# Kernel optimization log

Hardware: AMD Instinct MI355X
Metric: run time of the kernel (lower is better)

The kernel has to match this reference:

```python
import jax, jax.numpy as jnp
import numpy as np

G, NB, C, K, R, S = 5, 5, 64, 3, 8, 2   # n_groups, n_blocks, n_feats, kernel, reduction, scale
MOCO = 256


def setup_inputs() -> dict:
    key = jax.random.key(0)
    ks = iter(jax.random.split(key, 32))
    def rn(shape, s=0.02):
        return jax.random.normal(next(ks), shape, jnp.float32) * s
    return {
        "x": jax.random.normal(next(ks), (16, 3, 64, 64), jnp.float32),
        "k_v": jax.random.normal(next(ks), (16, MOCO), jnp.float32),
        "head_w": rn((C, 3, K, K)), "head_b": rn((C,)),
        "comp_w": rn((C, MOCO)),
        # DA_conv params, stacked over [group, block, which-of-2]
        "da_kw1": rn((G, NB, 2, C, C)),
        "da_kw2": rn((G, NB, 2, C * K * K, C)),
        "da_cw": rn((G, NB, 2, C, C)), "da_cb": rn((G, NB, 2, C)),
        "ca_w1": rn((G, NB, 2, C // R, C)), "ca_w2": rn((G, NB, 2, C, C // R)),
        # DAB plain 3x3 convs (conv1, conv2)
        "dab_cw": rn((G, NB, 2, C, C, K, K)), "dab_cb": rn((G, NB, 2, C)),
        # per-group tail conv, body tail conv, upsampler, final conv
        "grp_w": rn((G, C, C, K, K)), "grp_b": rn((G, C)),
        "body_w": rn((C, C, K, K)), "body_b": rn((C,)),
        "up_w": rn((C * S * S, C, K, K)), "up_b": rn((C * S * S,)),
        "tail_w": rn((3, C, K, K)), "tail_b": rn((3,)),
    }


def lrelu(x):
    return jax.nn.leaky_relu(x, 0.1)


def conv2d(x, w, b):
    p = (K - 1) // 2
    y = jax.lax.conv_general_dilated(x, w, (1, 1), [(p, p), (p, p)],
                                     dimension_numbers=("NCHW", "OIHW", "NCHW"))
    return y + b[None, :, None, None]


def da_conv(x, kv, kw1, kw2, cw, cb, caw1, caw2):
    # x: [B,C,H,W], kv: [B,C]
    B, Ch, H, W = x.shape
    # per-sample, per-channel dynamic KxK kernel (torch: groups=B*C depthwise conv)
    ker = (lrelu(kv @ kw1.T) @ kw2.T).reshape(B, Ch, K, K)
    p = (K - 1) // 2
    xp = jnp.pad(x, ((0, 0), (0, 0), (p, p), (p, p)))
    out = jnp.zeros_like(x)
    for i in range(K):
        for j in range(K):
            out = out + ker[:, :, i, j, None, None] * xp[:, :, i:i + H, j:j + W]
    out = lrelu(out)
    # 1x1 conv (with bias)
    out = jnp.einsum("bchw,oc->bohw", out, cw) + cb[None, :, None, None]
    # CA gate on kv (two bias-free 1x1 convs on 1x1 spatial == matmuls)
    att = jax.nn.sigmoid(lrelu(kv @ caw1.T) @ caw2.T)  # [B,C]
    return out + x * att[:, :, None, None]


def pixel_shuffle(t, r):
    B, Ct, H, W = t.shape
    c = Ct // (r * r)
    return t.reshape(B, c, r, r, H, W).transpose(0, 1, 4, 2, 5, 3).reshape(B, c, H * r, W * r)


def _forward(x, k_v, head_w, head_b, comp_w, da_kw1, da_kw2, da_cw, da_cb,
             ca_w1, ca_w2, dab_cw, dab_cb, grp_w, grp_b, body_w, body_b,
             up_w, up_b, tail_w, tail_b):
    kv = lrelu(k_v @ comp_w.T)            # compress: [B, C]
    x0 = conv2d(x, head_w, head_b)        # head
    res = x0
    for g in range(G):                    # DAGs
        gin = res
        for n in range(NB):               # DABs
            bin_ = res
            out = lrelu(da_conv(res, kv, da_kw1[g, n, 0], da_kw2[g, n, 0],
                                da_cw[g, n, 0], da_cb[g, n, 0], ca_w1[g, n, 0], ca_w2[g, n, 0]))
            out = lrelu(conv2d(out, dab_cw[g, n, 0], dab_cb[g, n, 0]))
            out = lrelu(da_conv(out, kv, da_kw1[g, n, 1], da_kw2[g, n, 1],
                                da_cw[g, n, 1], da_cb[g, n, 1], ca_w1[g, n, 1], ca_w2[g, n, 1]))
            res = conv2d(out, dab_cw[g, n, 1], dab_cb[g, n, 1]) + bin_
        res = conv2d(res, grp_w[g], grp_b[g]) + gin
    res = conv2d(res, body_w, body_b) + x0
    t = pixel_shuffle(conv2d(res, up_w, up_b), S)   # Upsampler (scale=2)
    return conv2d(t, tail_w, tail_b)


def reference(x, k_v, head_w, head_b, comp_w, da_kw1, da_kw2, da_cw, da_cb,
              ca_w1, ca_w2, dab_cw, dab_cb, grp_w, grp_b, body_w, body_b,
              up_w, up_b, tail_w, tail_b):
    return _forward(x, k_v, head_w, head_b, comp_w, da_kw1, da_kw2, da_cw, da_cb,
                    ca_w1, ca_w2, dab_cw, dab_cb, grp_w, grp_b, body_w, body_b,
                    up_w, up_b, tail_w, tail_b)
```

## Files before the change

kernel.cpp:

```cpp
#include <hip/hip_runtime.h>
#include <math.h>

#define DEV __device__ __forceinline__

DEV float lrelu_f(float v) { return v > 0.f ? v : 0.1f * v; }

DEV unsigned short f2bf(float f) {
    unsigned u = __builtin_bit_cast(unsigned, f);
    unsigned r = u + 0x7FFFu + ((u >> 16) & 1u);
    return (unsigned short)(r >> 16);
}

DEV float bf2f(unsigned short s) {
    return __builtin_bit_cast(float, (unsigned)s << 16);
}

typedef __attribute__((ext_vector_type(8))) short bh8;
typedef __attribute__((ext_vector_type(16))) float f16acc;

#define MFMA32(acc, a, b) acc = __builtin_amdgcn_mfma_f32_32x32x16_bf16(a, b, acc, 0, 0, 0)

__global__ void transpose_w(const float* __restrict__ src, float* __restrict__ dst,
                            int L, int O, int KK) {
    int idx = blockIdx.x * 256 + threadIdx.x;
    int tot = L * O * KK;
    if (idx >= tot) return;
    int l = idx / (O * KK);
    int r = idx - l * (O * KK);
    int o = r / KK;
    int k = r - o * KK;
    dst[((size_t)l * KK + k) * O + o] = src[idx];
}

__global__ void pack3x3(const float* __restrict__ src, unsigned short* __restrict__ dst, int L) {
    int idx = blockIdx.x * 256 + threadIdx.x;
    if (idx >= L * 4608) return;
    int l = idx / 4608;
    int r = idx - l * 4608;
    int c = r >> 7;
    int rr = r & 127;
    int nt = rr >> 6, lane = rr & 63;
    int o = nt * 32 + (lane & 31);
    int kg = lane >> 5;
    unsigned short v[8];
#pragma unroll
    for (int j = 0; j < 8; ++j) {
        int k = c * 16 + kg * 8 + j;
        int t = k >> 6, cin = k & 63;
        v[j] = f2bf(src[(((size_t)l * 64 + o) * 64 + cin) * 9 + t]);
    }
    uint4 u;
    u.x = v[0] | ((unsigned)v[1] << 16);
    u.y = v[2] | ((unsigned)v[3] << 16);
    u.z = v[4] | ((unsigned)v[5] << 16);
    u.w = v[6] | ((unsigned)v[7] << 16);
    *(uint4*)(dst + (size_t)idx * 8) = u;
}

__global__ void pack_da(const float* __restrict__ src, unsigned short* __restrict__ dst, int L) {
    int idx = blockIdx.x * 256 + threadIdx.x;
    if (idx >= L * 512) return;
    int l = idx >> 9;
    int r = idx & 511;
    int c = r >> 7;
    int rr = r & 127;
    int nt = rr >> 6, lane = rr & 63;
    int o = nt * 32 + (lane & 31);
    int kg = lane >> 5;
    unsigned short v[8];
#pragma unroll
    for (int j = 0; j < 8; ++j) {
        int cin = c * 16 + kg * 8 + j;
        v[j] = f2bf(src[((size_t)l * 64 + o) * 64 + cin]);
    }
    uint4 u;
    u.x = v[0] | ((unsigned)v[1] << 16);
    u.y = v[2] | ((unsigned)v[3] << 16);
    u.z = v[4] | ((unsigned)v[5] << 16);
    u.w = v[6] | ((unsigned)v[7] << 16);
    *(uint4*)(dst + (size_t)idx * 8) = u;
}

__global__ void pack_up(const float* __restrict__ src, unsigned short* __restrict__ dst) {
    int idx = blockIdx.x * 256 + threadIdx.x;
    if (idx >= 18432) return;
    int c = idx >> 9;
    int nt = (idx >> 6) & 7;
    int lane = idx & 63;
    int o = nt * 32 + (lane & 31);
    int kg = lane >> 5;
    unsigned short v[8];
#pragma unroll
    for (int j = 0; j < 8; ++j) {
        int k = c * 16 + kg * 8 + j;
        int t = k >> 6, cin = k & 63;
        v[j] = f2bf(src[((size_t)o * 64 + cin) * 9 + t]);
    }
    uint4 u;
    u.x = v[0] | ((unsigned)v[1] << 16);
    u.y = v[2] | ((unsigned)v[3] << 16);
    u.z = v[4] | ((unsigned)v[5] << 16);
    u.w = v[6] | ((unsigned)v[7] << 16);
    *(uint4*)(dst + (size_t)idx * 8) = u;
}

__global__ void pack_tail(const float* __restrict__ src, unsigned short* __restrict__ dst) {
    int idx = blockIdx.x * 256 + threadIdx.x;
    if (idx >= 2304) return;
    int c = idx >> 6;
    int lane = idx & 63;
    int o = lane & 31;
    int kg = lane >> 5;
    unsigned short v[8];
#pragma unroll
    for (int j = 0; j < 8; ++j) {
        int k = c * 16 + kg * 8 + j;
        int t = k >> 6, cin = k & 63;
        v[j] = (o < 3) ? f2bf(src[((size_t)o * 64 + cin) * 9 + t]) : (unsigned short)0;
    }
    uint4 u;
    u.x = v[0] | ((unsigned)v[1] << 16);
    u.y = v[2] | ((unsigned)v[3] << 16);
    u.z = v[4] | ((unsigned)v[5] << 16);
    u.w = v[6] | ((unsigned)v[7] << 16);
    *(uint4*)(dst + (size_t)idx * 8) = u;
}

__global__ void kv_kernel(const float* __restrict__ kvin, const float* __restrict__ comp_w,
                          float* __restrict__ kv) {
    int b = blockIdx.x, c = threadIdx.x;
    const float* a = kvin + b * 256;
    const float* w = comp_w + c * 256;
    float s = 0.f;
    for (int m = 0; m < 256; ++m) s += a[m] * w[m];
    kv[b * 64 + c] = lrelu_f(s);
}

__global__ void kerprep(const float* __restrict__ kv, const float* __restrict__ kw1,
                        const float* __restrict__ kw2, const float* __restrict__ caw1,
                        const float* __restrict__ caw2, float* __restrict__ ker_all,
                        float* __restrict__ att_all) {
    int l = blockIdx.x >> 4;
    int b = blockIdx.x & 15;
    int c = threadIdx.x;
    __shared__ float kvb[64];
    __shared__ float t1[64];
    __shared__ float a1[8];
    kvb[c] = kv[b * 64 + c];
    __syncthreads();
    {
        const float* w1 = kw1 + (size_t)l * 4096 + c * 64;
        float s = 0.f;
        for (int j = 0; j < 64; ++j) s += kvb[j] * w1[j];
        t1[c] = lrelu_f(s);
    }
    if (c < 8) {
        const float* cw1 = caw1 + (size_t)l * 512 + c * 64;
        float s = 0.f;
        for (int j = 0; j < 64; ++j) s += kvb[j] * cw1[j];
        a1[c] = lrelu_f(s);
    }
    __syncthreads();
    const float* w2 = kw2 + (size_t)l * 576 * 64;
    for (int t = 0; t < 9; ++t) {
        const float* row = w2 + (size_t)(c * 9 + t) * 64;
        float s = 0.f;
        for (int j = 0; j < 64; ++j) s += t1[j] * row[j];
        ker_all[(((size_t)l * 16 + b) * 9 + t) * 64 + c] = s;
    }
    {
        const float* c2 = caw2 + (size_t)l * 512 + c * 8;
        float s = 0.f;
        for (int r = 0; r < 8; ++r) s += a1[r] * c2[r];
        att_all[((size_t)l * 16 + b) * 64 + c] = 1.f / (1.f + expf(-s));
    }
}

__global__ __launch_bounds__(256) void head_conv(const float* __restrict__ x,
                                                 const float* __restrict__ wt,
                                                 const float* __restrict__ bias,
                                                 float* __restrict__ x0,
                                                 float* __restrict__ res,
                                                 unsigned short* __restrict__ resS) {
    int t = threadIdx.x;
    int co = t & 63, q = t >> 6;
    int bid = blockIdx.x;
    int b = bid >> 7;
    int rem = bid & 127;
    int y = rem >> 1;
    int xs = (rem & 1) * 32 + q * 8;

    float bv = bias[co];
    float acc[8];
#pragma unroll
    for (int p = 0; p < 8; ++p) acc[p] = bv;

    int coff[10];
    bool cok[10];
#pragma unroll
    for (int i = 0; i < 10; ++i) {
        int col = xs - 1 + i;
        cok[i] = (col >= 0) && (col < 64);
        coff[i] = cok[i] ? col : 0;
    }
    for (int cin = 0; cin < 3; ++cin) {
#pragma unroll
        for (int ky = 0; ky < 3; ++ky) {
            int row = y + ky - 1;
            bool rok = (row >= 0) && (row < 64);
            const float* rp = x + ((size_t)(b * 3 + cin) * 64 + (rok ? row : 0)) * 64;
            float v[10];
#pragma unroll
            for (int i = 0; i < 10; ++i) v[i] = (rok && cok[i]) ? rp[coff[i]] : 0.f;
            const float* wp = wt + ((cin * 3 + ky) * 3) * 64 + co;
            float w0 = wp[0], w1 = wp[64], w2 = wp[128];
#pragma unroll
            for (int p = 0; p < 8; ++p) acc[p] += w0 * v[p] + w1 * v[p + 1] + w2 * v[p + 2];
        }
    }
    size_t ob = (((size_t)b * 64 + y) * 64 + xs) * 64 + co;
#pragma unroll
    for (int p = 0; p < 8; ++p) {
        x0[ob + (size_t)p * 64] = acc[p];
        res[ob + (size_t)p * 64] = acc[p];
        resS[ob + (size_t)p * 64] = f2bf(acc[p]);
    }
}

__global__ __launch_bounds__(256, 2) void conv3x3_mfma(const unsigned short* __restrict__ in,
                                                       const unsigned short* __restrict__ wp,
                                                       const float* __restrict__ bias,
                                                       const float* __restrict__ residF,
                                                       float* __restrict__ outF,
                                                       unsigned short* __restrict__ outB,
                                                       int act) {
    __shared__ unsigned short sm[180 * 72];
    int tid = threadIdx.x;
    int bid = blockIdx.x;
    int b = bid >> 5;
    int rem = bid & 31;
    int ty = rem >> 2, tx = rem & 3;
    const unsigned short* inb = in + (size_t)b * 262144;

    int lane = tid & 63, w = tid >> 6;
    const unsigned short* bp = wp + (size_t)lane * 8;

    bh8 q0[6], q1[6];
#pragma unroll
    for (int i = 0; i < 6; ++i) {
        q0[i] = *(const bh8*)&bp[(size_t)i * 1024];
        q1[i] = *(const bh8*)&bp[(size_t)i * 1024 + 512];
    }

    for (int i = tid; i < 1440; i += 256) {
        int px = i >> 3, c8 = i & 7;
        int hy = px / 18, hx = px - hy * 18;
        int row = ty * 8 + hy - 1, col = tx * 16 + hx - 1;
        uint4 u = make_uint4(0u, 0u, 0u, 0u);
        if (row >= 0 && row < 64 && col >= 0 && col < 64)
            u = *(const uint4*)(inb + (((size_t)row * 64 + col) * 64 + c8 * 8));
        *(uint4*)&sm[px * 72 + c8 * 8] = u;
    }
    __syncthreads();

    int l31 = lane & 31, kg8 = (lane >> 5) * 8;
    int p0 = w * 32 + l31;
    int ly0 = p0 >> 4, lx0 = p0 & 15;

    f16acc a0 = {0,0,0,0,0,0,0,0,0,0,0,0,0,0,0,0};
    f16acc a1 = a0;

#pragma unroll
    for (int c = 0; c < 36; ++c) {
        int t = c >> 2, cc = c & 3;
        int tyt = t / 3, txt = t - tyt * 3;
        int base = ((ly0 + tyt) * 18 + lx0 + txt) * 72 + cc * 16 + kg8;
        bh8 A = *(const bh8*)&sm[base];
        bh8 B0 = q0[c % 6], B1 = q1[c % 6];
        if (c + 6 < 36) {
            q0[c % 6] = *(const bh8*)&bp[(size_t)(c + 6) * 1024];
            q1[c % 6] = *(const bh8*)&bp[(size_t)(c + 6) * 1024 + 512];
        }
        MFMA32(a0, A, B0);
        MFMA32(a1, A, B1);
    }

    float bias0 = bias[l31], bias1 = bias[32 + l31];
    int hi = lane >> 5;
    size_t outb = (size_t)b * 262144;
#pragma unroll
    for (int r = 0; r < 16; ++r) {
        int rowm = (r & 3) + 8 * (r >> 2) + 4 * hi;
        int m = w * 32 + rowm;
        int gy = ty * 8 + (m >> 4), gx = tx * 16 + (m & 15);
        size_t i0 = outb + (((size_t)gy * 64 + gx) * 64);
        float v0 = a0[r] + bias0, v1 = a1[r] + bias1;
        if (residF) {
            v0 += residF[i0 + l31];
            v1 += residF[i0 + 32 + l31];
        }
        if (act) { v0 = lrelu_f(v0); v1 = lrelu_f(v1); }
        if (outF) {
            outF[i0 + l31] = v0;
            outF[i0 + 32 + l31] = v1;
        }
        if (outB) {
            outB[i0 + l31] = f2bf(v0);
            outB[i0 + 32 + l31] = f2bf(v1);
        }
    }
}

__global__ __launch_bounds__(256, 2) void da_mfma(const unsigned short* __restrict__ in,
                                                  const unsigned short* __restrict__ wp,
                                                  const float* __restrict__ cb,
                                                  const float* __restrict__ kerT,
                                                  const float* __restrict__ attv,
                                                  unsigned short* __restrict__ out) {
    __shared__ unsigned short sm[180 * 72];
    __shared__ unsigned short mid[128 * 72];
    __shared__ unsigned short bds[4096];
    int tid = threadIdx.x;
    int bid = blockIdx.x;
    int b = bid >> 5;
    int rem = bid & 31;
    int ty = rem >> 2, tx = rem & 3;
    const unsigned short* inb = in + (size_t)b * 262144;

    for (int i = tid; i < 1440; i += 256) {
        int px = i >> 3, c8 = i & 7;
        int hy = px / 18, hx = px - hy * 18;
        int row = ty * 8 + hy - 1, col = tx * 16 + hx - 1;
        uint4 u = make_uint4(0u, 0u, 0u, 0u);
        if (row >= 0 && row < 64 && col >= 0 && col < 64)
            u = *(const uint4*)(inb + (((size_t)row * 64 + col) * 64 + c8 * 8));
        *(uint4*)&sm[px * 72 + c8 * 8] = u;
    }
#pragma unroll
    for (int i = 0; i < 2; ++i) {
        int idx = i * 256 + tid;
        *(uint4*)&bds[idx * 8] = *(const uint4*)&wp[idx * 8];
    }
    __syncthreads();

    {
        int c2 = tid & 31, q = tid >> 5;
        const float* kb = kerT + (size_t)b * 576 + 2 * c2;
        float ka[9], kbv[9];
#pragma unroll
        for (int t = 0; t < 9; ++t) {
            ka[t] = kb[t * 64];
            kbv[t] = kb[t * 64 + 1];
        }
        float m0[16], m1[16];
#pragma unroll
        for (int xx = 0; xx < 16; ++xx) { m0[xx] = 0.f; m1[xx] = 0.f; }
#pragma unroll
        for (int ky = 0; ky < 3; ++ky) {
            int hr = q + ky;
            float va[18], vb[18];
#pragma unroll
            for (int i = 0; i < 18; ++i) {
                unsigned u = *(const unsigned*)&sm[(hr * 18 + i) * 72 + 2 * c2];
                va[i] = bf2f((unsigned short)(u & 0xffffu));
                vb[i] = bf2f((unsigned short)(u >> 16));
            }
            float k0a = ka[ky * 3], k1a = ka[ky * 3 + 1], k2a = ka[ky * 3 + 2];
            float k0b = kbv[ky * 3], k1b = kbv[ky * 3 + 1], k2b = kbv[ky * 3 + 2];
#pragma unroll
            for (int xx = 0; xx < 16; ++xx) {
                m0[xx] += k0a * va[xx] + k1a * va[xx + 1] + k2a * va[xx + 2];
                m1[xx] += k0b * vb[xx] + k1b * vb[xx + 1] + k2b * vb[xx + 2];
            }
        }
#pragma unroll
        for (int xx = 0; xx < 16; ++xx) {
            unsigned u = (unsigned)f2bf(lrelu_f(m0[xx])) |
                         ((unsigned)f2bf(lrelu_f(m1[xx])) << 16);
            *(unsigned*)&mid[(q * 16 + xx) * 72 + 2 * c2] = u;
        }
    }
    __syncthreads();

    int lane = tid & 63, w = tid >> 6;
    int l31 = lane & 31, kg8 = (lane >> 5) * 8;
    int base = (w * 32 + l31) * 72 + kg8;

    f16acc a0 = {0,0,0,0,0,0,0,0,0,0,0,0,0,0,0,0};
    f16acc a1 = a0;
#pragma unroll
    for (int cc = 0; cc < 4; ++cc) {
        bh8 A = *(const bh8*)&mid[base + cc * 16];
        bh8 B0 = *(const bh8*)&bds[((cc * 2 + 0) * 64 + lane) * 8];
        bh8 B1 = *(const bh8*)&bds[((cc * 2 + 1) * 64 + lane) * 8];
        MFMA32(a0, A, B0);
        MFMA32(a1, A, B1);
    }

    float cb0 = cb[l31], cb1 = cb[32 + l31];
    float at0 = attv[b * 64 + l31], at1 = attv[b * 64 + 32 + l31];
    int hi = lane >> 5;
    size_t outb = (size_t)b * 262144;
#pragma unroll
    for (int r = 0; r < 16; ++r) {
        int rowm = (r & 3) + 8 * (r >> 2) + 4 * hi;
        int m = w * 32 + rowm;
        int gy = ty * 8 + (m >> 4), gx = tx * 16 + (m & 15);
        size_t i0 = outb + (((size_t)gy * 64 + gx) * 64);
        float v0 = a0[r] + cb0 + bf2f(in[i0 + l31]) * at0;
        float v1 = a1[r] + cb1 + bf2f(in[i0 + 32 + l31]) * at1;
        out[i0 + l31] = f2bf(lrelu_f(v0));
        out[i0 + 32 + l31] = f2bf(lrelu_f(v1));
    }
}

__global__ __launch_bounds__(256, 2) void up_mfma(const unsigned short* __restrict__ in,
                                                  const unsigned short* __restrict__ wp,
                                                  const float* __restrict__ bias,
                                                  unsigned short* __restrict__ shuf) {
    __shared__ unsigned short sm[100 * 72];
    int tid = threadIdx.x;
    int bid = blockIdx.x;
    int b = bid >> 6;
    int t6 = bid & 63;
    int ty = t6 >> 3, tx = t6 & 7;
    const unsigned short* inb = in + (size_t)b * 262144;

    int lane = tid & 63, w = tid >> 6;
    const unsigned short* bp = wp + (size_t)(w * 2) * 512 + (size_t)lane * 8;

    bh8 q0[4], q1[4];
#pragma unroll
    for (int i = 0; i < 4; ++i) {
        q0[i] = *(const bh8*)&bp[(size_t)i * 4096];
        q1[i] = *(const bh8*)&bp[(size_t)i * 4096 + 512];
    }

    for (int i = tid; i < 800; i += 256) {
        int px = i >> 3, c8 = i & 7;
        int hy = px / 10, hx = px - hy * 10;
        int row = ty * 8 + hy - 1, col = tx * 8 + hx - 1;
        uint4 u = make_uint4(0u, 0u, 0u, 0u);
        if (row >= 0 && row < 64 && col >= 0 && col < 64)
            u = *(const uint4*)(inb + (((size_t)row * 64 + col) * 64 + c8 * 8));
        *(uint4*)&sm[px * 72 + c8 * 8] = u;
    }
    __syncthreads();

    int l31 = lane & 31, kg8 = (lane >> 5) * 8;
    int ly0 = l31 >> 3, lx0 = l31 & 7;

    f16acc a00 = {0,0,0,0,0,0,0,0,0,0,0,0,0,0,0,0};
    f16acc a01 = a00, a10 = a00, a11 = a00;

#pragma unroll
    for (int c = 0; c < 36; ++c) {
        int t = c >> 2, cc = c & 3;
        int tyt = t / 3, txt = t - tyt * 3;
        int base0 = ((ly0 + tyt) * 10 + lx0 + txt) * 72 + cc * 16 + kg8;
        int base1 = base0 + 2880;
        bh8 A0 = *(const bh8*)&sm[base0];
        bh8 A1 = *(const bh8*)&sm[base1];
        bh8 B0 = q0[c % 4], B1 = q1[c % 4];
        if (c + 4 < 36) {
            q0[c % 4] = *(const bh8*)&bp[(size_t)(c + 4) * 4096];
            q1[c % 4] = *(const bh8*)&bp[(size_t)(c + 4) * 4096 + 512];
        }
        MFMA32(a00, A0, B0);
        MFMA32(a01, A0, B1);
        MFMA32(a10, A1, B0);
        MFMA32(a11, A1, B1);
    }

    int co0 = w * 64 + l31, co1 = co0 + 32;
    float bias0 = bias[co0], bias1 = bias[co1];
    int ch0 = co0 >> 2, r10 = (co0 >> 1) & 1, r20 = co0 & 1;
    int ch1 = co1 >> 2, r11 = (co1 >> 1) & 1, r21 = co1 & 1;
    int hi = lane >> 5;
#pragma unroll
    for (int r = 0; r < 16; ++r) {
        int rowm = (r & 3) + 8 * (r >> 2) + 4 * hi;
#pragma unroll
        for (int mt = 0; mt < 2; ++mt) {
            int m = mt * 32 + rowm;
            int y = ty * 8 + (m >> 3), x = tx * 8 + (m & 7);
            float va = (mt == 0) ? a00[r] : a10[r];
            float vb = (mt == 0) ? a01[r] : a11[r];
            shuf[(((size_t)b * 128 + 2 * y + r10) * 128 + 2 * x + r20) * 64 + ch0] = f2bf(va + bias0);
            shuf[(((size_t)b * 128 + 2 * y + r11) * 128 + 2 * x + r21) * 64 + ch1] = f2bf(vb + bias1);
        }
    }
}

__global__ __launch_bounds__(256) void tail_mfma(const unsigned short* __restrict__ shuf,
                                                 const unsigned short* __restrict__ wp,
                                                 const float* __restrict__ bias,
                                                 float* __restrict__ outp) {
    __shared__ unsigned short sm[324 * 72];
    int tid = threadIdx.x;
    int bid = blockIdx.x;
    int b = bid >> 6;
    int rem = bid & 63;
    int ty = rem >> 3, tx = rem & 7;
    const unsigned short* sb = shuf + (size_t)b * 128 * 128 * 64;

    for (int i = tid; i < 2592; i += 256) {
        int px = i >> 3, c8 = i & 7;
        int hy = px / 18, hx = px - hy * 18;
        int row = ty * 16 + hy - 1, col = tx * 16 + hx - 1;
        uint4 u = make_uint4(0u, 0u, 0u, 0u);
        if (row >= 0 && row < 128 && col >= 0 && col < 128)
            u = *(const uint4*)(sb + (((size_t)row * 128 + col) * 64 + c8 * 8));
        *(uint4*)&sm[px * 72 + c8 * 8] = u;
    }
    __syncthreads();

    int lane = tid & 63, w = tid >> 6;
    int l31 = lane & 31, kg8 = (lane >> 5) * 8;
    int mbase = w * 64;
    int p0 = mbase + l31;
    int ly0 = p0 >> 4, lx0 = p0 & 15;

    f16acc a0 = {0,0,0,0,0,0,0,0,0,0,0,0,0,0,0,0};
    f16acc a1 = a0;

#pragma unroll
    for (int t = 0; t < 9; ++t) {
        int tyt = t / 3, txt = t - tyt * 3;
        int base0 = ((ly0 + tyt) * 18 + lx0 + txt) * 72 + kg8;
        int base1 = base0 + 2592;
#pragma unroll
        for (int cc = 0; cc < 4; ++cc) {
            int c = t * 4 + cc;
            bh8 A0 = *(const bh8*)&sm[base0 + cc * 16];
            bh8 A1 = *(const bh8*)&sm[base1 + cc * 16];
            bh8 B = *(const bh8*)&wp[((size_t)c * 64 + lane) * 8];
            MFMA32(a0, A0, B);
            MFMA32(a1, A1, B);
        }
    }

    if (l31 < 3) {
        float bv = bias[l31];
        int hi = lane >> 5;
        size_t ob = ((size_t)b * 3 + l31) * 16384;
#pragma unroll
        for (int r = 0; r < 16; ++r) {
            int rowm = (r & 3) + 8 * (r >> 2) + 4 * hi;
            int m0 = mbase + rowm;
            int gy0 = ty * 16 + (m0 >> 4), gx0 = tx * 16 + (m0 & 15);
            outp[ob + (size_t)gy0 * 128 + gx0] = a0[r] + bv;
            int m1 = m0 + 32;
            int gy1 = ty * 16 + (m1 >> 4), gx1 = tx * 16 + (m1 & 15);
            outp[ob + (size_t)gy1 * 128 + gx1] = a1[r] + bv;
        }
    }
}

extern "C" void kernel_launch(void* const* d_in, const int* in_sizes, int n_in,
                              void* d_out, int out_size, void* d_ws, size_t ws_size,
                              hipStream_t stream) {
    const float* x      = (const float*)d_in[0];
    const float* k_v    = (const float*)d_in[1];
    const float* head_w = (const float*)d_in[2];
    const float* head_b = (const float*)d_in[3];
    const float* comp_w = (const float*)d_in[4];
    const float* da_kw1 = (const float*)d_in[5];
    const float* da_kw2 = (const float*)d_in[6];
    const float* da_cw  = (const float*)d_in[7];
    const float* da_cb  = (const float*)d_in[8];
    const float* ca_w1  = (const float*)d_in[9];
    const float* ca_w2  = (const float*)d_in[10];
    const float* dab_cw = (const float*)d_in[11];
    const float* dab_cb = (const float*)d_in[12];
    const float* grp_w  = (const float*)d_in[13];
    const float* grp_b  = (const float*)d_in[14];
    const float* body_w = (const float*)d_in[15];
    const float* body_b = (const float*)d_in[16];
    const float* up_w   = (const float*)d_in[17];
    const float* up_b   = (const float*)d_in[18];
    const float* tail_w = (const float*)d_in[19];
    const float* tail_b = (const float*)d_in[20];

    char* base = (char*)d_ws;
    auto alloc = [&](size_t bytes) -> char* {
        char* p = base;
        base += (bytes + 255) & ~(size_t)255;
        return p;
    };
    unsigned short* wp_dab  = (unsigned short*)alloc((size_t)50 * 36864 * 2);
    unsigned short* wp_grp  = (unsigned short*)alloc((size_t)5 * 36864 * 2);
    unsigned short* wp_body = (unsigned short*)alloc((size_t)36864 * 2);
    unsigned short* wp_up   = (unsigned short*)alloc((size_t)147456 * 2);
    unsigned short* wp_da   = (unsigned short*)alloc((size_t)50 * 4096 * 2);
    unsigned short* wp_tail = (unsigned short*)alloc((size_t)18432 * 2);
    float* wT_head = (float*)alloc(1728 * 4);
    float* kvbuf   = (float*)alloc(1024 * 4);
    float* ker_all = (float*)alloc((size_t)460800 * 4);
    float* att_all = (float*)alloc((size_t)51200 * 4);
    const size_t ACT = (size_t)16 * 64 * 64 * 64;
    float* x0 = (float*)alloc(ACT * 4);
    float* rA = (float*)alloc(ACT * 4);
    float* rB = (float*)alloc(ACT * 4);
    float* rC = (float*)alloc(ACT * 4);
    unsigned short* sA = (unsigned short*)alloc(ACT * 2);
    unsigned short* sB = (unsigned short*)alloc(ACT * 2);
    unsigned short* sC = (unsigned short*)alloc(ACT * 2);
    unsigned short* t0 = (unsigned short*)alloc(ACT * 2);
    unsigned short* t1 = (unsigned short*)alloc(ACT * 2);
    unsigned short* shuf = (unsigned short*)alloc((size_t)16 * 128 * 128 * 64 * 2);

    pack3x3<<<900, 256, 0, stream>>>(dab_cw, wp_dab, 50);
    pack3x3<<<90, 256, 0, stream>>>(grp_w, wp_grp, 5);
    pack3x3<<<18, 256, 0, stream>>>(body_w, wp_body, 1);
    pack_da<<<100, 256, 0, stream>>>(da_cw, wp_da, 50);
    pack_up<<<72, 256, 0, stream>>>(up_w, wp_up);
    pack_tail<<<9, 256, 0, stream>>>(tail_w, wp_tail);
    transpose_w<<<7, 256, 0, stream>>>(head_w, wT_head, 1, 64, 27);

    kv_kernel<<<16, 64, 0, stream>>>(k_v, comp_w, kvbuf);
    kerprep<<<800, 64, 0, stream>>>(kvbuf, da_kw1, da_kw2, ca_w1, ca_w2, ker_all, att_all);

    head_conv<<<2048, 256, 0, stream>>>(x, wT_head, head_b, x0, rA, sA);

    for (int g = 0; g < 5; ++g) {
        float* curF = rA;
        unsigned short* curS = sA;
        for (int n = 0; n < 5; ++n) {
            int l0 = (g * 5 + n) * 2, l1 = l0 + 1;
            da_mfma<<<512, 256, 0, stream>>>(curS, wp_da + (size_t)l0 * 4096,
                                             da_cb + (size_t)l0 * 64, ker_all + (size_t)l0 * 9216,
                                             att_all + (size_t)l0 * 1024, t0);
            conv3x3_mfma<<<512, 256, 0, stream>>>(t0, wp_dab + (size_t)l0 * 36864,
                                                  dab_cb + (size_t)l0 * 64, nullptr,
                                                  nullptr, t1, 1);
            da_mfma<<<512, 256, 0, stream>>>(t1, wp_da + (size_t)l1 * 4096,
                                             da_cb + (size_t)l1 * 64, ker_all + (size_t)l1 * 9216,
                                             att_all + (size_t)l1 * 1024, t0);
            float* outF = (curF == rB) ? rC : rB;
            unsigned short* outS = (curS == sB) ? sC : sB;
            conv3x3_mfma<<<512, 256, 0, stream>>>(t0, wp_dab + (size_t)l1 * 36864,
                                                  dab_cb + (size_t)l1 * 64, curF,
                                                  outF, outS, 0);
            curF = outF;
            curS = outS;
        }
        conv3x3_mfma<<<512, 256, 0, stream>>>(curS, wp_grp + (size_t)g * 36864,
                                              grp_b + (size_t)g * 64, rA, rC, sC, 0);
        float* tf = rA; rA = rC; rC = tf;
        unsigned short* ts = sA; sA = sC; sC = ts;
    }
    conv3x3_mfma<<<512, 256, 0, stream>>>(sA, wp_body, body_b, x0, nullptr, t0, 0);

    up_mfma<<<1024, 256, 0, stream>>>(t0, wp_up, up_b, shuf);
    tail_mfma<<<1024, 256, 0, stream>>>(shuf, wp_tail, tail_b, (float*)d_out);
}
```

Measured before the change: 1.534 ms.

## Fuse dynamic depthwise DA conv with following 3x3 conv into one kernel

Merges the da_mfma kernel and the subsequent conv3x3_mfma into a single dab_mfma kernel. It loads a 2-pixel halo tile and computes the DA output over an 18x10 halo region in shared memory, then runs the 3x3 MFMA conv directly from LDS. This removes one global write and read of the intermediate bf16 activation and one launch per DA/conv pair. The cost is redundant halo computation (180 vs 128 pixels), larger LDS use and more registers for the prefetched weights.

```diff
diff --git a/kernel.cpp b/kernel.cpp
--- a/kernel.cpp
+++ b/kernel.cpp
@@ -311,15 +311,19 @@
     }
 }
 
-__global__ __launch_bounds__(256, 2) void da_mfma(const unsigned short* __restrict__ in,
-                                                  const unsigned short* __restrict__ wp,
-                                                  const float* __restrict__ cb,
-                                                  const float* __restrict__ kerT,
-                                                  const float* __restrict__ attv,
-                                                  unsigned short* __restrict__ out) {
-    __shared__ unsigned short sm[180 * 72];
-    __shared__ unsigned short mid[128 * 72];
-    __shared__ unsigned short bds[4096];
+__global__ __launch_bounds__(256, 2) void dab_mfma(const unsigned short* __restrict__ in,
+                                                   const unsigned short* __restrict__ wda,
+                                                   const float* __restrict__ cb,
+                                                   const float* __restrict__ kerT,
+                                                   const float* __restrict__ attv,
+                                                   const unsigned short* __restrict__ wconv,
+                                                   const float* __restrict__ cbias,
+                                                   const float* __restrict__ residF,
+                                                   float* __restrict__ outF,
+                                                   unsigned short* __restrict__ outB,
+                                                   int act) {
+    __shared__ unsigned short sin_[240 * 72];
+    __shared__ unsigned short mid[192 * 72];
     int tid = threadIdx.x;
     int bid = blockIdx.x;
     int b = bid >> 5;
@@ -327,19 +331,24 @@
     int ty = rem >> 2, tx = rem & 3;
     const unsigned short* inb = in + (size_t)b * 262144;
 
-    for (int i = tid; i < 1440; i += 256) {
+    int lane = tid & 63, w = tid >> 6;
+    int l31 = lane & 31, kg8 = (lane >> 5) * 8, hi = lane >> 5;
+
+    bh8 dB0[4], dB1[4];
+#pragma unroll
+    for (int cc = 0; cc < 4; ++cc) {
+        dB0[cc] = *(const bh8*)&wda[((size_t)(cc * 2 + 0) * 64 + lane) * 8];
+        dB1[cc] = *(const bh8*)&wda[((size_t)(cc * 2 + 1) * 64 + lane) * 8];
+    }
+
+    for (int i = tid; i < 1920; i += 256) {
         int px = i >> 3, c8 = i & 7;
-        int hy = px / 18, hx = px - hy * 18;
-        int row = ty * 8 + hy - 1, col = tx * 16 + hx - 1;
+        int hy = px / 20, hx = px - hy * 20;
+        int row = ty * 8 + hy - 2, col = tx * 16 + hx - 2;
         uint4 u = make_uint4(0u, 0u, 0u, 0u);
         if (row >= 0 && row < 64 && col >= 0 && col < 64)
             u = *(const uint4*)(inb + (((size_t)row * 64 + col) * 64 + c8 * 8));
-        *(uint4*)&sm[px * 72 + c8 * 8] = u;
-    }
-#pragma unroll
-    for (int i = 0; i < 2; ++i) {
-        int idx = i * 256 + tid;
-        *(uint4*)&bds[idx * 8] = *(const uint4*)&wp[idx * 8];
+        *(uint4*)&sin_[px * 72 + c8 * 8] = u;
     }
     __syncthreads();
 
@@ -352,54 +361,104 @@
             ka[t] = kb[t * 64];
             kbv[t] = kb[t * 64 + 1];
         }
-        float m0[16], m1[16];
-#pragma unroll
-        for (int xx = 0; xx < 16; ++xx) { m0[xx] = 0.f; m1[xx] = 0.f; }
-#pragma unroll
-        for (int ky = 0; ky < 3; ++ky) {
-            int hr = q + ky;
-            float va[18], vb[18];
-#pragma unroll
-            for (int i = 0; i < 18; ++i) {
-                unsigned u = *(const unsigned*)&sm[(hr * 18 + i) * 72 + 2 * c2];
-                va[i] = bf2f((unsigned short)(u & 0xffffu));
-                vb[i] = bf2f((unsigned short)(u >> 16));
+#pragma unroll
+        for (int rr = 0; rr < 2; ++rr) {
+            int my = (rr == 0) ? q : 8 + q;
+            if (rr == 1 && q >= 2) break;
+            float m0[18], m1[18];
+#pragma unroll
+            for (int xx = 0; xx < 18; ++xx) { m0[xx] = 0.f; m1[xx] = 0.f; }
+#pragma unroll
+            for (int ky = 0; ky < 3; ++ky) {
+                int sr = my + ky;
+                float va[20], vb[20];
+#pragma unroll
+                for (int i = 0; i < 20; ++i) {
+                    unsigned u = *(const unsigned*)&sin_[(sr * 20 + i) * 72 + 2 * c2];
+                    va[i] = bf2f((unsigned short)(u & 0xffffu));
+                    vb[i] = bf2f((unsigned short)(u >> 16));
+                }
+                float k0a = ka[ky * 3], k1a = ka[ky * 3 + 1], k2a = ka[ky * 3 + 2];
+                float k0b = kbv[ky * 3], k1b = kbv[ky * 3 + 1], k2b = kbv[ky * 3 + 2];
+#pragma unroll
+                for (int xx = 0; xx < 18; ++xx) {
+                    m0[xx] += k0a * va[xx] + k1a * va[xx + 1] + k2a * va[xx + 2];
+                    m1[xx] += k0b * vb[xx] + k1b * vb[xx + 1] + k2b * vb[xx + 2];
+                }
             }
-            float k0a = ka[ky * 3], k1a = ka[ky * 3 + 1], k2a = ka[ky * 3 + 2];
-            float k0b = kbv[ky * 3], k1b = kbv[ky * 3 + 1], k2b = kbv[ky * 3 + 2];
-#pragma unroll
-            for (int xx = 0; xx < 16; ++xx) {
-                m0[xx] += k0a * va[xx] + k1a * va[xx + 1] + k2a * va[xx + 2];
-                m1[xx] += k0b * vb[xx] + k1b * vb[xx + 1] + k2b * vb[xx + 2];
+#pragma unroll
+            for (int xx = 0; xx < 18; ++xx) {
+                unsigned u = (unsigned)f2bf(lrelu_f(m0[xx])) |
+                             ((unsigned)f2bf(lrelu_f(m1[xx])) << 16);
+                *(unsigned*)&mid[(my * 18 + xx) * 72 + 2 * c2] = u;
             }
         }
-#pragma unroll
-        for (int xx = 0; xx < 16; ++xx) {
-            unsigned u = (unsigned)f2bf(lrelu_f(m0[xx])) |
-                         ((unsigned)f2bf(lrelu_f(m1[xx])) << 16);
-            *(unsigned*)&mid[(q * 16 + xx) * 72 + 2 * c2] = u;
-        }
     }
     __syncthreads();
 
-    int lane = tid & 63, w = tid >> 6;
-    int l31 = lane & 31, kg8 = (lane >> 5) * 8;
-    int base = (w * 32 + l31) * 72 + kg8;
-
-    f16acc a0 = {0,0,0,0,0,0,0,0,0,0,0,0,0,0,0,0};
-    f16acc a1 = a0;
-#pragma unroll
-    for (int cc = 0; cc < 4; ++cc) {
-        bh8 A = *(const bh8*)&mid[base + cc * 16];
-        bh8 B0 = *(const bh8*)&bds[((cc * 2 + 0) * 64 + lane) * 8];
-        bh8 B1 = *(const bh8*)&bds[((cc * 2 + 1) * 64 + lane) * 8];
-        MFMA32(a0, A, B0);
-        MFMA32(a1, A, B1);
-    }
-
-    float cb0 = cb[l31], cb1 = cb[32 + l31];
-    float at0 = attv[b * 64 + l31], at1 = attv[b * 64 + 32 + l31];
-    int hi = lane >> 5;
+    {
+        float cb0 = cb[l31], cb1 = cb[32 + l31];
+        float at0 = attv[b * 64 + l31], at1 = attv[b * 64 + 32 + l31];
+        for (int mt = w; mt < 6; mt += 4) {
+            f16acc a0 = {0,0,0,0,0,0,0,0,0,0,0,0,0,0,0,0};
+            f16acc a1 = a0;
+#pragma unroll
+            for (int cc = 0; cc < 4; ++cc) {
+                bh8 A = *(const bh8*)&mid[(mt * 32 + l31) * 72 + cc * 16 + kg8];
+                MFMA32(a0, A, dB0[cc]);
+                MFMA32(a1, A, dB1[cc]);
+            }
+#pragma unroll
+            for (int r = 0; r < 16; ++r) {
+                int rowm = (r & 3) + 8 * (r >> 2) + 4 * hi;
+                int px = mt * 32 + rowm;
+                if (px < 180) {
+                    int my = px / 18, mx = px - my * 18;
+                    int gy = ty * 8 + my - 1, gx = tx * 16 + mx - 1;
+                    bool ok = (gy >= 0) && (gy < 64) && (gx >= 0) && (gx < 64);
+                    int spx = (my + 1) * 20 + (mx + 1);
+                    float i0v = bf2f(sin_[spx * 72 + l31]);
+                    float i1v = bf2f(sin_[spx * 72 + 32 + l31]);
+                    float v0 = lrelu_f(a0[r] + cb0 + i0v * at0);
+                    float v1 = lrelu_f(a1[r] + cb1 + i1v * at1);
+                    mid[px * 72 + l31] = ok ? f2bf(v0) : (unsigned short)0;
+                    mid[px * 72 + 32 + l31] = ok ? f2bf(v1) : (unsigned short)0;
+                }
+            }
+        }
+    }
+
+    const unsigned short* bp = wconv + (size_t)lane * 8;
+    bh8 q0[6], q1[6];
+#pragma unroll
+    for (int i = 0; i < 6; ++i) {
+        q0[i] = *(const bh8*)&bp[(size_t)i * 1024];
+        q1[i] = *(const bh8*)&bp[(size_t)i * 1024 + 512];
+    }
+    __syncthreads();
+
+    int p0 = w * 32 + l31;
+    int ly0 = p0 >> 4, lx0 = p0 & 15;
+
+    f16acc c0 = {0,0,0,0,0,0,0,0,0,0,0,0,0,0,0,0};
+    f16acc c1 = c0;
+
+#pragma unroll
+    for (int c = 0; c < 36; ++c) {
+        int t = c >> 2, cc = c & 3;
+        int tyt = t / 3, txt = t - tyt * 3;
+        int base = ((ly0 + tyt) * 18 + lx0 + txt) * 72 + cc * 16 + kg8;
+        bh8 A = *(const bh8*)&mid[base];
+        bh8 B0 = q0[c % 6], B1 = q1[c % 6];
+        if (c + 6 < 36) {
+            q0[c % 6] = *(const bh8*)&bp[(size_t)(c + 6) * 1024];
+            q1[c % 6] = *(const bh8*)&bp[(size_t)(c + 6) * 1024 + 512];
+        }
+        MFMA32(c0, A, B0);
+        MFMA32(c1, A, B1);
+    }
+
+    float bias0 = cbias[l31], bias1 = cbias[32 + l31];
     size_t outb = (size_t)b * 262144;
 #pragma unroll
     for (int r = 0; r < 16; ++r) {
@@ -407,10 +466,20 @@
         int m = w * 32 + rowm;
         int gy = ty * 8 + (m >> 4), gx = tx * 16 + (m & 15);
         size_t i0 = outb + (((size_t)gy * 64 + gx) * 64);
-        float v0 = a0[r] + cb0 + bf2f(in[i0 + l31]) * at0;
-        float v1 = a1[r] + cb1 + bf2f(in[i0 + 32 + l31]) * at1;
-        out[i0 + l31] = f2bf(lrelu_f(v0));
-        out[i0 + 32 + l31] = f2bf(lrelu_f(v1));
+        float v0 = c0[r] + bias0, v1 = c1[r] + bias1;
+        if (residF) {
+            v0 += residF[i0 + l31];
+            v1 += residF[i0 + 32 + l31];
+        }
+        if (act) { v0 = lrelu_f(v0); v1 = lrelu_f(v1); }
+        if (outF) {
+            outF[i0 + l31] = v0;
+            outF[i0 + 32 + l31] = v1;
+        }
+        if (outB) {
+            outB[i0 + l31] = f2bf(v0);
+            outB[i0 + 32 + l31] = f2bf(v1);
+        }
     }
 }
 
@@ -606,7 +675,6 @@
     unsigned short* sA = (unsigned short*)alloc(ACT * 2);
     unsigned short* sB = (unsigned short*)alloc(ACT * 2);
     unsigned short* sC = (unsigned short*)alloc(ACT * 2);
-    unsigned short* t0 = (unsigned short*)alloc(ACT * 2);
     unsigned short* t1 = (unsigned short*)alloc(ACT * 2);
     unsigned short* shuf = (unsigned short*)alloc((size_t)16 * 128 * 128 * 64 * 2);
 
@@ -628,20 +696,24 @@
         unsigned short* curS = sA;
         for (int n = 0; n < 5; ++n) {
             int l0 = (g * 5 + n) * 2, l1 = l0 + 1;
-            da_mfma<<<512, 256, 0, stream>>>(curS, wp_da + (size_t)l0 * 4096,
-                                             da_cb + (size_t)l0 * 64, ker_all + (size_t)l0 * 9216,
-                                             att_all + (size_t)l0 * 1024, t0);
-            conv3x3_mfma<<<512, 256, 0, stream>>>(t0, wp_dab + (size_t)l0 * 36864,
-                                                  dab_cb + (size_t)l0 * 64, nullptr,
-                                                  nullptr, t1, 1);
-            da_mfma<<<512, 256, 0, stream>>>(t1, wp_da + (size_t)l1 * 4096,
-                                             da_cb + (size_t)l1 * 64, ker_all + (size_t)l1 * 9216,
-                                             att_all + (size_t)l1 * 1024, t0);
+            dab_mfma<<<512, 256, 0, stream>>>(curS,
+                                              wp_da + (size_t)l0 * 4096,
+                                              da_cb + (size_t)l0 * 64,
+                                              ker_all + (size_t)l0 * 9216,
+                                              att_all + (size_t)l0 * 1024,
+                                              wp_dab + (size_t)l0 * 36864,
+                                              dab_cb + (size_t)l0 * 64,
+                                              nullptr, nullptr, t1, 1);
             float* outF = (curF == rB) ? rC : rB;
             unsigned short* outS = (curS == sB) ? sC : sB;
-            conv3x3_mfma<<<512, 256, 0, stream>>>(t0, wp_dab + (size_t)l1 * 36864,
-                                                  dab_cb + (size_t)l1 * 64, curF,
-                                                  outF, outS, 0);
+            dab_mfma<<<512, 256, 0, stream>>>(t1,
+                                              wp_da + (size_t)l1 * 4096,
+                                              da_cb + (size_t)l1 * 64,
+                                              ker_all + (size_t)l1 * 9216,
+                                              att_all + (size_t)l1 * 1024,
+                                              wp_dab + (size_t)l1 * 36864,
+                                              dab_cb + (size_t)l1 * 64,
+                                              curF, outF, outS, 0);
             curF = outF;
             curS = outS;
         }
@@ -650,8 +722,8 @@
         float* tf = rA; rA = rC; rC = tf;
         unsigned short* ts = sA; sA = sC; sC = ts;
     }
-    conv3x3_mfma<<<512, 256, 0, stream>>>(sA, wp_body, body_b, x0, nullptr, t0, 0);
-
-    up_mfma<<<1024, 256, 0, stream>>>(t0, wp_up, up_b, shuf);
+    conv3x3_mfma<<<512, 256, 0, stream>>>(sA, wp_body, body_b, x0, nullptr, t1, 0);
+
+    up_mfma<<<1024, 256, 0, stream>>>(t1, wp_up, up_b, shuf);
     tail_mfma<<<1024, 256, 0, stream>>>(shuf, wp_tail, tail_b, (float*)d_out);
 }
```

Result: no change. 1.524 ms (-0.6%).
